# Performance work log

Measured on AMD Instinct MI355X. Metric: run time of the kernel, lower is better.

Reference implementation:

```python
import jax, jax.numpy as jnp
import numpy as np

D_MODEL = 1024
N_HEAD = 16
L, B = 2048, 2


def setup_inputs() -> dict:
    key = jax.random.key(0)
    ks = jax.random.split(key, 11)
    inp = {
        "q": jax.random.normal(ks[0], (L, B, D_MODEL), dtype=jnp.float32),
        "k": jax.random.normal(ks[1], (L, B, D_MODEL), dtype=jnp.float32),
        "v": jax.random.normal(ks[2], (L, B, D_MODEL), dtype=jnp.float32),
        "sph": jax.random.uniform(ks[3], (B, N_HEAD, L, L), dtype=jnp.float32),
        "mask": jax.random.randint(ks[4], (B, L, L), 0, 2, dtype=jnp.int32),
        # learned params (torch Linear stores W of shape [out, in]; y = x @ W.T)
        "Wq": jax.random.normal(ks[5], (D_MODEL, D_MODEL), dtype=jnp.float32) * (1.0 / np.sqrt(D_MODEL)),
        "Wk": jax.random.normal(ks[6], (D_MODEL, D_MODEL), dtype=jnp.float32) * (1.0 / np.sqrt(D_MODEL)),
        "Wv": jax.random.normal(ks[7], (D_MODEL, D_MODEL), dtype=jnp.float32) * (1.0 / np.sqrt(D_MODEL)),
        "Wfc": jax.random.normal(ks[8], (D_MODEL, D_MODEL), dtype=jnp.float32) * (1.0 / np.sqrt(D_MODEL)),
        "gamma": jnp.ones((D_MODEL,), dtype=jnp.float32),
        "beta": jnp.zeros((D_MODEL,), dtype=jnp.float32),
    }
    return inp


def reference(q, k, v, sph, mask, Wq, Wk, Wv, Wfc, gamma, beta):
    # q, k, v: [L, B, D]  ->  batch-first [B, L, D]
    n_head = N_HEAD
    Lq, Bb, D = q.shape
    d_k = D // n_head
    x_q = jnp.transpose(q, (1, 0, 2))
    x_k = jnp.transpose(k, (1, 0, 2))
    x_v = jnp.transpose(v, (1, 0, 2))
    residual = x_q  # [B, L, D]

    # projections (no bias), split heads: [B, H, L, d_k]
    qh = (x_q @ Wq.T).reshape(Bb, Lq, n_head, d_k).transpose(0, 2, 1, 3)
    kh = (x_k @ Wk.T).reshape(Bb, Lq, n_head, d_k).transpose(0, 2, 1, 3)
    vh = (x_v @ Wv.T).reshape(Bb, Lq, n_head, d_k).transpose(0, 2, 1, 3)

    scale = jnp.asarray(d_k, qh.dtype) ** 0.5
    attn = jnp.einsum('bhqd,bhkd->bhqk', qh / scale, kh)
    attn = attn * sph                                   # spatial decay modulation
    attn = jnp.where(mask[:, None, :, :] == 0, jnp.asarray(-1e9, attn.dtype), attn)
    p_attn = jax.nn.softmax(attn, axis=-1)              # dropout is identity in eval

    out = jnp.einsum('bhqk,bhkd->bhqd', p_attn, vh)     # [B, H, L, d_k]
    out = out.transpose(0, 2, 1, 3).reshape(Bb, Lq, D)
    out = out @ Wfc.T + residual                        # fc (no bias) + residual

    # LayerNorm(eps=1e-6)
    mu = jnp.mean(out, axis=-1, keepdims=True)
    var = jnp.var(out, axis=-1, keepdims=True)
    out = (out - mu) * jax.lax.rsqrt(var + 1e-6) * gamma + beta

    return jnp.transpose(out, (1, 0, 2)), p_attn
```

## Files before the change

### kernel.cpp

```cpp
#include <hip/hip_runtime.h>
#include <hip/hip_bf16.h>

#define LL 2048
#define BB 2
#define DD 1024
#define HH 16
#define DKk 64

typedef __attribute__((ext_vector_type(8))) short s8v;
typedef __attribute__((ext_vector_type(8))) unsigned short u8v;
typedef __attribute__((ext_vector_type(4))) float f4v;

__device__ __forceinline__ ushort f2b(float f){
  union { __hip_bfloat16 h; ushort u; } c; c.h = __float2bfloat16(f); return c.u;
}
__device__ __forceinline__ float b2f(ushort u){
  union { __hip_bfloat16 h; ushort u; } c; c.u = u; return __bfloat162float(c.h);
}

__global__ __launch_bounds__(256) void pack_x_kernel(
    const float* __restrict__ q, const float* __restrict__ k, const float* __restrict__ v,
    ushort* __restrict__ xq, ushort* __restrict__ xk, ushort* __restrict__ xv){
  int t = blockIdx.x*256 + threadIdx.x;
  int m = t >> 7;
  int dc = (t & 127) << 3;
  int b = m >> 11, l = m & (LL-1);
  size_t src = ((size_t)(l*BB + b) << 10) + dc;
  size_t dst = ((size_t)m << 10) + dc;
  #pragma unroll
  for (int i=0;i<3;++i){
    const float* ss = (i==0)?q:(i==1)?k:v;
    ushort* dd = (i==0)?xq:(i==1)?xk:xv;
    float4 a = *(const float4*)(ss+src);
    float4 bb = *(const float4*)(ss+src+4);
    u8v o;
    o[0]=f2b(a.x); o[1]=f2b(a.y); o[2]=f2b(a.z); o[3]=f2b(a.w);
    o[4]=f2b(bb.x);o[5]=f2b(bb.y);o[6]=f2b(bb.z);o[7]=f2b(bb.w);
    *(u8v*)(dd+dst) = o;
  }
}

__global__ __launch_bounds__(256) void pack_w_kernel(
    const float* __restrict__ Wq, const float* __restrict__ Wk,
    const float* __restrict__ Wv, const float* __restrict__ Wfc,
    ushort* __restrict__ wb){
  int t = blockIdx.x*256 + threadIdx.x;
  int which = t >> 17;
  size_t idx = (size_t)(t & 131071) << 3;
  const float* s = (which==0)?Wq:(which==1)?Wk:(which==2)?Wv:Wfc;
  float4 a = *(const float4*)(s+idx);
  float4 b4 = *(const float4*)(s+idx+4);
  u8v o;
  o[0]=f2b(a.x);o[1]=f2b(a.y);o[2]=f2b(a.z);o[3]=f2b(a.w);
  o[4]=f2b(b4.x);o[5]=f2b(b4.y);o[6]=f2b(b4.z);o[7]=f2b(b4.w);
  *(u8v*)(wb + ((size_t)which<<20) + idx) = o;
}

__device__ __forceinline__ void gemm_body(
    const ushort* __restrict__ A, const ushort* __restrict__ W,
    ushort* __restrict__ outb, float* __restrict__ outf, const float* __restrict__ resid,
    int mode, float scale){
  __shared__ ushort As[4096];
  __shared__ ushort Bs[4096];
  int tid = threadIdx.x;
  int w = tid>>6, lane = tid&63, lane15 = lane&15, g = lane>>4;
  int m0 = blockIdx.y<<7, n0 = blockIdx.x<<7;
  int wr = w>>1, wc = w&1;
  f4v z4 = {0.f,0.f,0.f,0.f};
  f4v acc[4][4];
  #pragma unroll
  for (int i=0;i<4;++i)
    #pragma unroll
    for (int j=0;j<4;++j) acc[i][j] = z4;

  int f0 = tid, f1 = 256 + tid;
  int r0 = f0>>2, c0 = (f0&3)<<3;
  int r1 = f1>>2, c1 = (f1&3)<<3;
  for (int k0=0; k0<1024; k0+=32){
    *(s8v*)&As[(r0<<5)+c0] = *(const s8v*)&A[((size_t)(m0+r0)<<10) + k0 + c0];
    *(s8v*)&As[(r1<<5)+c1] = *(const s8v*)&A[((size_t)(m0+r1)<<10) + k0 + c1];
    *(s8v*)&Bs[(r0<<5)+c0] = *(const s8v*)&W[((size_t)(n0+r0)<<10) + k0 + c0];
    *(s8v*)&Bs[(r1<<5)+c1] = *(const s8v*)&W[((size_t)(n0+r1)<<10) + k0 + c1];
    __syncthreads();
    s8v af[4], bf_[4];
    #pragma unroll
    for (int mi=0;mi<4;++mi) af[mi] = *(s8v*)&As[((wr*64 + mi*16 + lane15)<<5) + (g<<3)];
    #pragma unroll
    for (int ni=0;ni<4;++ni) bf_[ni] = *(s8v*)&Bs[((wc*64 + ni*16 + lane15)<<5) + (g<<3)];
    #pragma unroll
    for (int mi=0;mi<4;++mi)
      #pragma unroll
      for (int ni=0;ni<4;++ni)
        acc[mi][ni] = __builtin_amdgcn_mfma_f32_16x16x32_bf16(af[mi], bf_[ni], acc[mi][ni], 0,0,0);
    __syncthreads();
  }
  #pragma unroll
  for (int mi=0;mi<4;++mi){
    #pragma unroll
    for (int ni=0;ni<4;++ni){
      int mbase = m0 + wr*64 + mi*16 + (g<<2);
      int ncol  = n0 + wc*64 + ni*16 + lane15;
      if (mode==0){
        int b=mbase>>11, h=ncol>>6, j=ncol&63;
        size_t o = (((size_t)(b*HH+h)*LL + (mbase&2047))<<6) + j;
        #pragma unroll
        for (int r=0;r<4;++r) outb[o + ((size_t)r<<6)] = f2b(acc[mi][ni][r]*scale);
      } else if (mode==2){
        int b=mbase>>11, h=ncol>>6, j=ncol&63;
        ushort4 pk = make_ushort4(f2b(acc[mi][ni][0]), f2b(acc[mi][ni][1]),
                                  f2b(acc[mi][ni][2]), f2b(acc[mi][ni][3]));
        *(ushort4*)&outb[(((size_t)(b*HH+h)*DKk + j)<<11) + (mbase&2047)] = pk;
      } else {
        int b=mbase>>11, l2=mbase&2047;
        #pragma unroll
        for (int r=0;r<4;++r)
          outf[((size_t)(mbase+r)<<10)+ncol] =
              acc[mi][ni][r] + resid[((size_t)((l2+r)*BB + b)<<10) + ncol];
      }
    }
  }
}

__global__ __launch_bounds__(256) void gemm_qkv_kernel(
    const ushort* __restrict__ xq, const ushort* __restrict__ xk, const ushort* __restrict__ xv,
    const ushort* __restrict__ wb, ushort* __restrict__ Qh, ushort* __restrict__ Kh, ushort* __restrict__ Vt){
  int z = blockIdx.z;
  const ushort* A = (z==0)?xq:(z==1)?xk:xv;
  const ushort* W = wb + ((size_t)z<<20);
  ushort* outb = (z==0)?Qh:(z==1)?Kh:Vt;
  int mode = (z==2)?2:0;
  float scale = (z==0)?0.125f:1.0f;
  gemm_body(A, W, outb, nullptr, nullptr, mode, scale);
}

__global__ __launch_bounds__(256) void gemm_fc_kernel(
    const ushort* __restrict__ ao, const ushort* __restrict__ wfc,
    const float* __restrict__ resid, float* __restrict__ fco){
  gemm_body(ao, wfc, nullptr, fco, resid, 3, 1.0f);
}

__global__ __launch_bounds__(1024) void attn_kernel(
    const ushort* __restrict__ Qh, const ushort* __restrict__ Kh, const ushort* __restrict__ Vt,
    const float* __restrict__ sph, const int* __restrict__ mask,
    float* __restrict__ p_out, ushort* __restrict__ attn_out){
  extern __shared__ char smem[];
  float* pbuf   = (float*)(smem + 65536);
  float* redsum = (float*)(smem + 65536 + 13056);
  int tid = threadIdx.x, w = tid>>6, lane = tid&63, lane15 = lane&15, g = lane>>4;
  int bid = blockIdx.x;
  int qt = bid & 127, h = (bid>>7)&15, b = bid>>11;
  int q0 = qt<<4;
  size_t bh = (size_t)b*HH + h;

  const ushort* Qbase = Qh + ((bh*LL + q0 + lane15)<<6) + (g<<3);
  s8v qa0 = *(const s8v*)Qbase;
  s8v qa1 = *(const s8v*)(Qbase + 32);
  #pragma unroll
  for (int cc=0; cc<8; ++cc){
    int c = (w<<3) + cc;
    const ushort* Kb = Kh + ((bh*LL + (c<<4) + lane15)<<6) + (g<<3);
    s8v kb0 = *(const s8v*)Kb;
    s8v kb1 = *(const s8v*)(Kb + 32);
    f4v cacc = {0.f,0.f,0.f,0.f};
    cacc = __builtin_amdgcn_mfma_f32_16x16x32_bf16(qa0, kb0, cacc, 0,0,0);
    cacc = __builtin_amdgcn_mfma_f32_16x16x32_bf16(qa1, kb1, cacc, 0,0,0);
    int colb = ((c<<4) + lane15) << 1;
    #pragma unroll
    for (int r=0;r<4;++r){
      int row = (g<<2)+r;
      *(ushort*)(smem + (row<<12) + (colb ^ ((row&7)<<4))) = f2b(cacc[r]);
    }
  }
  __syncthreads();

  int row = w;
  int qrow = q0 + row;
  const float* sph_r = sph + ((bh*LL + qrow)<<11);
  const int*  msk_r  = mask + (((size_t)b*LL + qrow)<<11);
  int rswz = (row&7)<<4;
  char* Srow = smem + (row<<12);
  float sum = 0.f;
  #pragma unroll
  for (int c2=0;c2<4;++c2){
    int col = (lane<<3) + (c2<<9);
    int boff = (col<<1) ^ rswz;
    s8v sv = *(s8v*)(Srow + boff);
    float4 p0 = *(const float4*)(sph_r + col);
    float4 p1 = *(const float4*)(sph_r + col + 4);
    int4 mk0 = *(const int4*)(msk_r + col);
    int4 mk1 = *(const int4*)(msk_r + col + 4);
    float e[8];
    e[0] = mk0.x ? __expf(b2f((ushort)sv[0])*p0.x) : 0.f;
    e[1] = mk0.y ? __expf(b2f((ushort)sv[1])*p0.y) : 0.f;
    e[2] = mk0.z ? __expf(b2f((ushort)sv[2])*p0.z) : 0.f;
    e[3] = mk0.w ? __expf(b2f((ushort)sv[3])*p0.w) : 0.f;
    e[4] = mk1.x ? __expf(b2f((ushort)sv[4])*p1.x) : 0.f;
    e[5] = mk1.y ? __expf(b2f((ushort)sv[5])*p1.y) : 0.f;
    e[6] = mk1.z ? __expf(b2f((ushort)sv[6])*p1.z) : 0.f;
    e[7] = mk1.w ? __expf(b2f((ushort)sv[7])*p1.w) : 0.f;
    u8v ov;
    #pragma unroll
    for (int j=0;j<8;++j){ ushort ue = f2b(e[j]); sum += b2f(ue); ov[j] = ue; }
    *(u8v*)(Srow + boff) = ov;
  }
  #pragma unroll
  for (int off=1; off<64; off<<=1) sum += __shfl_xor(sum, off, 64);
  if (lane==0) redsum[row] = sum;

  float inv = 1.0f / sum;
  float* prow_p = p_out + ((bh*LL + qrow)<<11);
  #pragma unroll
  for (int c2=0;c2<4;++c2){
    int col = (lane<<3) + (c2<<9);
    s8v sv = *(s8v*)(Srow + ((col<<1) ^ rswz));
    float4 o0, o1;
    o0.x=b2f((ushort)sv[0])*inv; o0.y=b2f((ushort)sv[1])*inv;
    o0.z=b2f((ushort)sv[2])*inv; o0.w=b2f((ushort)sv[3])*inv;
    o1.x=b2f((ushort)sv[4])*inv; o1.y=b2f((ushort)sv[5])*inv;
    o1.z=b2f((ushort)sv[6])*inv; o1.w=b2f((ushort)sv[7])*inv;
    *(float4*)(prow_p + col) = o0;
    *(float4*)(prow_p + col + 4) = o1;
  }
  __syncthreads();

  int ds = w & 3, kq = w >> 2;
  f4v oacc = {0.f,0.f,0.f,0.f};
  const ushort* Vb = Vt + ((bh*DKk + (ds<<4) + lane15)<<11) + (kq<<9) + (g<<3);
  char* Sa = smem + (lane15<<12);
  int aswz = (lane15&7)<<4;
  #pragma unroll
  for (int it=0; it<16; ++it){
    s8v pa = *(s8v*)(Sa + (((kq<<10) + (it<<6) + (g<<4)) ^ aswz));
    s8v vb = *(const s8v*)(Vb + (it<<5));
    oacc = __builtin_amdgcn_mfma_f32_16x16x32_bf16(pa, vb, oacc, 0,0,0);
  }
  if (kq){
    float* pp = pbuf + ((kq-1)*1088);
    #pragma unroll
    for (int r=0;r<4;++r) pp[((g<<2)+r)*68 + (ds<<4) + lane15] = oacc[r];
  }
  __syncthreads();
  if (kq==0){
    #pragma unroll
    for (int p=0;p<3;++p){
      float* pp = pbuf + p*1088;
      #pragma unroll
      for (int r=0;r<4;++r) oacc[r] += pp[((g<<2)+r)*68 + (ds<<4) + lane15];
    }
    #pragma unroll
    for (int r=0;r<4;++r){
      int qr = (g<<2)+r;
      float val = oacc[r] / redsum[qr];
      attn_out[((size_t)(b*LL + q0 + qr)<<10) + (h<<6) + (ds<<4) + lane15] = f2b(val);
    }
  }
}

__global__ __launch_bounds__(256) void ln_kernel(const float* __restrict__ fc,
    const float* __restrict__ gamma, const float* __restrict__ beta, float* __restrict__ out){
  __shared__ float rs[4], rq[4];
  int m = blockIdx.x, tid = threadIdx.x;
  int d0 = tid<<2;
  float4 x = *(const float4*)(fc + ((size_t)m<<10) + d0);
  float s = x.x+x.y+x.z+x.w;
  float sq = x.x*x.x+x.y*x.y+x.z*x.z+x.w*x.w;
  #pragma unroll
  for (int off=32; off; off>>=1){ s += __shfl_xor(s,off,64); sq += __shfl_xor(sq,off,64); }
  if ((tid&63)==0){ rs[tid>>6]=s; rq[tid>>6]=sq; }
  __syncthreads();
  float ts = rs[0]+rs[1]+rs[2]+rs[3];
  float tq = rq[0]+rq[1]+rq[2]+rq[3];
  float mu = ts*(1.0f/1024.0f);
  float var = tq*(1.0f/1024.0f) - mu*mu;
  float rr = rsqrtf(var + 1e-6f);
  float4 gm = *(const float4*)(gamma + d0);
  float4 bt = *(const float4*)(beta + d0);
  float4 y;
  y.x=(x.x-mu)*rr*gm.x+bt.x;
  y.y=(x.y-mu)*rr*gm.y+bt.y;
  y.z=(x.z-mu)*rr*gm.z+bt.z;
  y.w=(x.w-mu)*rr*gm.w+bt.w;
  int b=m>>11, l2=m&2047;
  *(float4*)(out + ((size_t)(l2*BB+b)<<10) + d0) = y;
}

extern "C" void kernel_launch(void* const* d_in, const int* in_sizes, int n_in,
                              void* d_out, int out_size, void* d_ws, size_t ws_size,
                              hipStream_t stream){
  const float* q    = (const float*)d_in[0];
  const float* k    = (const float*)d_in[1];
  const float* v    = (const float*)d_in[2];
  const float* sph  = (const float*)d_in[3];
  const int*   mask = (const int*)d_in[4];
  const float* Wq   = (const float*)d_in[5];
  const float* Wk   = (const float*)d_in[6];
  const float* Wv   = (const float*)d_in[7];
  const float* Wfc  = (const float*)d_in[8];
  const float* gamma= (const float*)d_in[9];
  const float* beta = (const float*)d_in[10];
  float* outp  = (float*)d_out;
  float* p_out = outp + 4194304;

  char* ws = (char*)d_ws;
  ushort* xq  = (ushort*)(ws);
  ushort* xk  = (ushort*)(ws + 8388608);
  ushort* xv  = (ushort*)(ws + 16777216);
  ushort* wb  = (ushort*)(ws + 25165824);
  ushort* Qh  = (ushort*)(ws + 33554432);
  ushort* Kh  = (ushort*)(ws + 41943040);
  ushort* Vt  = (ushort*)(ws + 50331648);
  ushort* ao  = (ushort*)(ws + 58720256);
  float*  fco = (float*)(ws + 67108864);

  pack_x_kernel<<<2048,256,0,stream>>>(q,k,v,xq,xk,xv);
  pack_w_kernel<<<2048,256,0,stream>>>(Wq,Wk,Wv,Wfc,wb);
  gemm_qkv_kernel<<<dim3(8,32,3),256,0,stream>>>(xq,xk,xv,wb,Qh,Kh,Vt);
  attn_kernel<<<4096,1024,78784,stream>>>(Qh,Kh,Vt,sph,mask,p_out,ao);
  gemm_fc_kernel<<<dim3(8,32),256,0,stream>>>(ao, wb + 3145728, q, fco);
  ln_kernel<<<4096,256,0,stream>>>(fco, gamma, beta, outp);
}
```

Measured before the change: 553.6 us.

## Pipeline attention over key chunks with bit-packed mask and smaller LDS

Restructures the attention kernel to process keys in 8 chunks of 256 with a double-buffered LDS score tile. The next sph chunk is prefetched with inline asm loads while QK^T, exp and PV MFMAs run per chunk, which cuts LDS from about 77KB to about 29KB so more blocks can be resident. The int32 mask is packed into bits by a merged pack kernel, reducing the mask bytes the attention kernel reads. p_attn is written with nontemporal stores. The cost is two barriers per chunk and hand-placed waitcnt asm that must stay correct.

Measured after the change: 569.0 us. 1.03x slower.

```diff
diff --git a/kernel.cpp b/kernel.cpp
--- a/kernel.cpp
+++ b/kernel.cpp
@@ -17,43 +17,58 @@
 __device__ __forceinline__ float b2f(ushort u){
   union { __hip_bfloat16 h; ushort u; } c; c.u = u; return __bfloat162float(c.h);
 }
-
-__global__ __launch_bounds__(256) void pack_x_kernel(
+__device__ __forceinline__ void nts4(float* p, f4v v){ __builtin_nontemporal_store(v, (f4v*)p); }
+
+__global__ __launch_bounds__(256) void pack_all_kernel(
     const float* __restrict__ q, const float* __restrict__ k, const float* __restrict__ v,
-    ushort* __restrict__ xq, ushort* __restrict__ xk, ushort* __restrict__ xv){
-  int t = blockIdx.x*256 + threadIdx.x;
-  int m = t >> 7;
-  int dc = (t & 127) << 3;
-  int b = m >> 11, l = m & (LL-1);
-  size_t src = ((size_t)(l*BB + b) << 10) + dc;
-  size_t dst = ((size_t)m << 10) + dc;
-  #pragma unroll
-  for (int i=0;i<3;++i){
-    const float* ss = (i==0)?q:(i==1)?k:v;
-    ushort* dd = (i==0)?xq:(i==1)?xk:xv;
-    float4 a = *(const float4*)(ss+src);
-    float4 bb = *(const float4*)(ss+src+4);
-    u8v o;
-    o[0]=f2b(a.x); o[1]=f2b(a.y); o[2]=f2b(a.z); o[3]=f2b(a.w);
-    o[4]=f2b(bb.x);o[5]=f2b(bb.y);o[6]=f2b(bb.z);o[7]=f2b(bb.w);
-    *(u8v*)(dd+dst) = o;
-  }
-}
-
-__global__ __launch_bounds__(256) void pack_w_kernel(
     const float* __restrict__ Wq, const float* __restrict__ Wk,
     const float* __restrict__ Wv, const float* __restrict__ Wfc,
-    ushort* __restrict__ wb){
-  int t = blockIdx.x*256 + threadIdx.x;
-  int which = t >> 17;
-  size_t idx = (size_t)(t & 131071) << 3;
-  const float* s = (which==0)?Wq:(which==1)?Wk:(which==2)?Wv:Wfc;
-  float4 a = *(const float4*)(s+idx);
-  float4 b4 = *(const float4*)(s+idx+4);
-  u8v o;
-  o[0]=f2b(a.x);o[1]=f2b(a.y);o[2]=f2b(a.z);o[3]=f2b(a.w);
-  o[4]=f2b(b4.x);o[5]=f2b(b4.y);o[6]=f2b(b4.z);o[7]=f2b(b4.w);
-  *(u8v*)(wb + ((size_t)which<<20) + idx) = o;
+    const int* __restrict__ mask,
+    ushort* __restrict__ xq, ushort* __restrict__ xk, ushort* __restrict__ xv,
+    ushort* __restrict__ wb, unsigned* __restrict__ mbits2){
+  int blk = blockIdx.x;
+  if (blk < 2048){
+    int t = blk*256 + threadIdx.x;
+    int m = t >> 7;
+    int dc = (t & 127) << 3;
+    int b = m >> 11, l = m & (LL-1);
+    size_t src = ((size_t)(l*BB + b) << 10) + dc;
+    size_t dst = ((size_t)m << 10) + dc;
+    #pragma unroll
+    for (int i=0;i<3;++i){
+      const float* ss = (i==0)?q:(i==1)?k:v;
+      ushort* dd = (i==0)?xq:(i==1)?xk:xv;
+      float4 a = *(const float4*)(ss+src);
+      float4 bb = *(const float4*)(ss+src+4);
+      u8v o;
+      o[0]=f2b(a.x); o[1]=f2b(a.y); o[2]=f2b(a.z); o[3]=f2b(a.w);
+      o[4]=f2b(bb.x);o[5]=f2b(bb.y);o[6]=f2b(bb.z);o[7]=f2b(bb.w);
+      *(u8v*)(dd+dst) = o;
+    }
+  } else if (blk < 4096){
+    int t = (blk-2048)*256 + threadIdx.x;
+    int which = t >> 17;
+    size_t idx = (size_t)(t & 131071) << 3;
+    const float* s = (which==0)?Wq:(which==1)?Wk:(which==2)?Wv:Wfc;
+    float4 a = *(const float4*)(s+idx);
+    float4 b4 = *(const float4*)(s+idx+4);
+    u8v o;
+    o[0]=f2b(a.x);o[1]=f2b(a.y);o[2]=f2b(a.z);o[3]=f2b(a.w);
+    o[4]=f2b(b4.x);o[5]=f2b(b4.y);o[6]=f2b(b4.z);o[7]=f2b(b4.w);
+    *(u8v*)(wb + ((size_t)which<<20) + idx) = o;
+  } else {
+    int t = (blk-4096)*256 + threadIdx.x;
+    int rowg = t >> 6, lane = t & 63;
+    const int* mrow = mask + ((size_t)rowg<<11) + (lane<<2);
+    unsigned mw = 0;
+    #pragma unroll
+    for (int ct=0; ct<8; ++ct){
+      int4 a = *(const int4*)(mrow + (ct<<8));
+      unsigned nib = (a.x&1) | ((a.y&1)<<1) | ((a.z&1)<<2) | ((a.w&1)<<3);
+      mw |= nib << (ct*4);
+    }
+    mbits2[((size_t)rowg<<6) + lane] = mw;
+  }
 }
 
 __device__ __forceinline__ void gemm_body(
@@ -139,111 +154,112 @@
   gemm_body(ao, wfc, nullptr, fco, resid, 3, 1.0f);
 }
 
-__global__ __launch_bounds__(1024) void attn_kernel(
+__global__ __launch_bounds__(1024, 4) void attn_kernel(
     const ushort* __restrict__ Qh, const ushort* __restrict__ Kh, const ushort* __restrict__ Vt,
-    const float* __restrict__ sph, const int* __restrict__ mask,
+    const float* __restrict__ sph, const unsigned* __restrict__ mbits2,
     float* __restrict__ p_out, ushort* __restrict__ attn_out){
   extern __shared__ char smem[];
-  float* pbuf   = (float*)(smem + 65536);
-  float* redsum = (float*)(smem + 65536 + 13056);
+  float* pbuf   = (float*)(smem + 16384);
+  float* redsum = (float*)(smem + 16384 + 13056);
   int tid = threadIdx.x, w = tid>>6, lane = tid&63, lane15 = lane&15, g = lane>>4;
   int bid = blockIdx.x;
   int qt = bid & 127, h = (bid>>7)&15, b = bid>>11;
   int q0 = qt<<4;
   size_t bh = (size_t)b*HH + h;
+  int qrow = q0 + w;
+
+  const float* sph_r = sph + ((bh*LL + qrow)<<11) + (lane<<2);
+  unsigned mw = mbits2[(((size_t)b*LL + qrow)<<6) + lane];
 
   const ushort* Qbase = Qh + ((bh*LL + q0 + lane15)<<6) + (g<<3);
   s8v qa0 = *(const s8v*)Qbase;
   s8v qa1 = *(const s8v*)(Qbase + 32);
-  #pragma unroll
-  for (int cc=0; cc<8; ++cc){
-    int c = (w<<3) + cc;
-    const ushort* Kb = Kh + ((bh*LL + (c<<4) + lane15)<<6) + (g<<3);
-    s8v kb0 = *(const s8v*)Kb;
-    s8v kb1 = *(const s8v*)(Kb + 32);
+
+  int rswz = (w&7)<<4;
+  int aswz = (lane15&7)<<4;
+  int ds = w & 3, kg = w >> 2;
+  float sum = 0.f;
+  f4v sp0, sp1;
+  ushort4 ev[8];
+  f4v oacc = {0.f,0.f,0.f,0.f};
+
+  asm volatile("global_load_dwordx4 %0, %1, off" : "=v"(sp0) : "v"(sph_r));
+
+  #pragma unroll
+  for (int ct=0; ct<8; ++ct){
+    if (ct<7){
+      const float* pn = sph_r + ((ct+1)<<8);
+      if (ct&1) asm volatile("global_load_dwordx4 %0, %1, off" : "=v"(sp0) : "v"(pn));
+      else      asm volatile("global_load_dwordx4 %0, %1, off" : "=v"(sp1) : "v"(pn));
+    }
+
+    const ushort* Kp = Kh + ((bh*LL + (ct<<8) + (w<<4) + lane15)<<6) + (g<<3);
+    s8v kb0 = *(const s8v*)Kp;
+    s8v kb1 = *(const s8v*)(Kp + 32);
     f4v cacc = {0.f,0.f,0.f,0.f};
     cacc = __builtin_amdgcn_mfma_f32_16x16x32_bf16(qa0, kb0, cacc, 0,0,0);
     cacc = __builtin_amdgcn_mfma_f32_16x16x32_bf16(qa1, kb1, cacc, 0,0,0);
-    int colb = ((c<<4) + lane15) << 1;
+    char* Sb = smem + ((ct&1)<<13);
+    int colb = ((w<<4) + lane15)<<1;
     #pragma unroll
     for (int r=0;r<4;++r){
-      int row = (g<<2)+r;
-      *(ushort*)(smem + (row<<12) + (colb ^ ((row&7)<<4))) = f2b(cacc[r]);
-    }
+      int ri = (g<<2)+r;
+      *(ushort*)(Sb + (ri<<9) + (colb ^ ((ri&7)<<4))) = f2b(cacc[r]);
+    }
+    __syncthreads();
+
+    f4v spv;
+    if (ct&1){ asm volatile("s_waitcnt vmcnt(0)" : "+v"(sp1)); spv = sp1; }
+    else     { asm volatile("s_waitcnt vmcnt(0)" : "+v"(sp0)); spv = sp0; }
+    __builtin_amdgcn_sched_barrier(0);
+
+    char* Srow = Sb + (w<<9);
+    int boff = (lane<<3) ^ rswz;
+    ushort4 sv = *(ushort4*)(Srow + boff);
+    unsigned m4 = mw >> (ct*4);
+    float e0 = (m4&1) ? __expf(b2f(sv.x)*spv[0]) : 0.f;
+    float e1 = (m4&2) ? __expf(b2f(sv.y)*spv[1]) : 0.f;
+    float e2 = (m4&4) ? __expf(b2f(sv.z)*spv[2]) : 0.f;
+    float e3 = (m4&8) ? __expf(b2f(sv.w)*spv[3]) : 0.f;
+    sum += (e0+e1)+(e2+e3);
+    ushort4 eb = make_ushort4(f2b(e0), f2b(e1), f2b(e2), f2b(e3));
+    ev[ct] = eb;
+    *(ushort4*)(Srow + boff) = eb;
+    __syncthreads();
+
+    const ushort* Vb = Vt + ((bh*DKk + (ds<<4) + lane15)<<11) + (ct<<8) + (kg<<6) + (g<<3);
+    s8v vb0 = *(const s8v*)Vb;
+    s8v vb1 = *(const s8v*)(Vb + 32);
+    char* Sa = Sb + (lane15<<9);
+    s8v pa0 = *(s8v*)(Sa + (((kg<<7) + (g<<4)) ^ aswz));
+    s8v pa1 = *(s8v*)(Sa + (((kg<<7) + 64 + (g<<4)) ^ aswz));
+    oacc = __builtin_amdgcn_mfma_f32_16x16x32_bf16(pa0, vb0, oacc, 0,0,0);
+    oacc = __builtin_amdgcn_mfma_f32_16x16x32_bf16(pa1, vb1, oacc, 0,0,0);
+  }
+
+  #pragma unroll
+  for (int off=1; off<64; off<<=1) sum += __shfl_xor(sum, off, 64);
+  if (lane==0) redsum[w] = sum;
+  float inv = 1.0f / sum;
+  float* prow = p_out + ((bh*LL + qrow)<<11) + (lane<<2);
+  #pragma unroll
+  for (int ct=0;ct<8;++ct){
+    f4v o;
+    o[0]=b2f(ev[ct].x)*inv; o[1]=b2f(ev[ct].y)*inv;
+    o[2]=b2f(ev[ct].z)*inv; o[3]=b2f(ev[ct].w)*inv;
+    nts4(prow + (ct<<8), o);
+  }
+
+  if (kg){
+    float* pp = pbuf + (kg-1)*1088;
+    #pragma unroll
+    for (int r=0;r<4;++r) pp[((g<<2)+r)*68 + (ds<<4) + lane15] = oacc[r];
   }
   __syncthreads();
-
-  int row = w;
-  int qrow = q0 + row;
-  const float* sph_r = sph + ((bh*LL + qrow)<<11);
-  const int*  msk_r  = mask + (((size_t)b*LL + qrow)<<11);
-  int rswz = (row&7)<<4;
-  char* Srow = smem + (row<<12);
-  float sum = 0.f;
-  #pragma unroll
-  for (int c2=0;c2<4;++c2){
-    int col = (lane<<3) + (c2<<9);
-    int boff = (col<<1) ^ rswz;
-    s8v sv = *(s8v*)(Srow + boff);
-    float4 p0 = *(const float4*)(sph_r + col);
-    float4 p1 = *(const float4*)(sph_r + col + 4);
-    int4 mk0 = *(const int4*)(msk_r + col);
-    int4 mk1 = *(const int4*)(msk_r + col + 4);
-    float e[8];
-    e[0] = mk0.x ? __expf(b2f((ushort)sv[0])*p0.x) : 0.f;
-    e[1] = mk0.y ? __expf(b2f((ushort)sv[1])*p0.y) : 0.f;
-    e[2] = mk0.z ? __expf(b2f((ushort)sv[2])*p0.z) : 0.f;
-    e[3] = mk0.w ? __expf(b2f((ushort)sv[3])*p0.w) : 0.f;
-    e[4] = mk1.x ? __expf(b2f((ushort)sv[4])*p1.x) : 0.f;
-    e[5] = mk1.y ? __expf(b2f((ushort)sv[5])*p1.y) : 0.f;
-    e[6] = mk1.z ? __expf(b2f((ushort)sv[6])*p1.z) : 0.f;
-    e[7] = mk1.w ? __expf(b2f((ushort)sv[7])*p1.w) : 0.f;
-    u8v ov;
-    #pragma unroll
-    for (int j=0;j<8;++j){ ushort ue = f2b(e[j]); sum += b2f(ue); ov[j] = ue; }
-    *(u8v*)(Srow + boff) = ov;
-  }
-  #pragma unroll
-  for (int off=1; off<64; off<<=1) sum += __shfl_xor(sum, off, 64);
-  if (lane==0) redsum[row] = sum;
-
-  float inv = 1.0f / sum;
-  float* prow_p = p_out + ((bh*LL + qrow)<<11);
-  #pragma unroll
-  for (int c2=0;c2<4;++c2){
-    int col = (lane<<3) + (c2<<9);
-    s8v sv = *(s8v*)(Srow + ((col<<1) ^ rswz));
-    float4 o0, o1;
-    o0.x=b2f((ushort)sv[0])*inv; o0.y=b2f((ushort)sv[1])*inv;
-    o0.z=b2f((ushort)sv[2])*inv; o0.w=b2f((ushort)sv[3])*inv;
-    o1.x=b2f((ushort)sv[4])*inv; o1.y=b2f((ushort)sv[5])*inv;
-    o1.z=b2f((ushort)sv[6])*inv; o1.w=b2f((ushort)sv[7])*inv;
-    *(float4*)(prow_p + col) = o0;
-    *(float4*)(prow_p + col + 4) = o1;
-  }
-  __syncthreads();
-
-  int ds = w & 3, kq = w >> 2;
-  f4v oacc = {0.f,0.f,0.f,0.f};
-  const ushort* Vb = Vt + ((bh*DKk + (ds<<4) + lane15)<<11) + (kq<<9) + (g<<3);
-  char* Sa = smem + (lane15<<12);
-  int aswz = (lane15&7)<<4;
-  #pragma unroll
-  for (int it=0; it<16; ++it){
-    s8v pa = *(s8v*)(Sa + (((kq<<10) + (it<<6) + (g<<4)) ^ aswz));
-    s8v vb = *(const s8v*)(Vb + (it<<5));
-    oacc = __builtin_amdgcn_mfma_f32_16x16x32_bf16(pa, vb, oacc, 0,0,0);
-  }
-  if (kq){
-    float* pp = pbuf + ((kq-1)*1088);
-    #pragma unroll
-    for (int r=0;r<4;++r) pp[((g<<2)+r)*68 + (ds<<4) + lane15] = oacc[r];
-  }
-  __syncthreads();
-  if (kq==0){
-    #pragma unroll
-    for (int p=0;p<3;++p){
-      float* pp = pbuf + p*1088;
+  if (kg==0){
+    #pragma unroll
+    for (int p3=0;p3<3;++p3){
+      float* pp = pbuf + p3*1088;
       #pragma unroll
       for (int r=0;r<4;++r) oacc[r] += pp[((g<<2)+r)*68 + (ds<<4) + lane15];
     }
@@ -311,11 +327,11 @@
   ushort* Vt  = (ushort*)(ws + 50331648);
   ushort* ao  = (ushort*)(ws + 58720256);
   float*  fco = (float*)(ws + 67108864);
-
-  pack_x_kernel<<<2048,256,0,stream>>>(q,k,v,xq,xk,xv);
-  pack_w_kernel<<<2048,256,0,stream>>>(Wq,Wk,Wv,Wfc,wb);
+  unsigned* mbits2 = (unsigned*)(ws + 83886080);
+
+  pack_all_kernel<<<5120,256,0,stream>>>(q,k,v,Wq,Wk,Wv,Wfc,mask,xq,xk,xv,wb,mbits2);
   gemm_qkv_kernel<<<dim3(8,32,3),256,0,stream>>>(xq,xk,xv,wb,Qh,Kh,Vt);
-  attn_kernel<<<4096,1024,78784,stream>>>(Qh,Kh,Vt,sph,mask,p_out,ao);
+  attn_kernel<<<4096,1024,29504,stream>>>(Qh,Kh,Vt,sph,mbits2,p_out,ao);
   gemm_fc_kernel<<<dim3(8,32),256,0,stream>>>(ao, wb + 3145728, q, fco);
   ln_kernel<<<4096,256,0,stream>>>(fco, gamma, beta, outp);
 }
```
